# Optimization experiments

Hardware: AMD Instinct MI355X
Metric: run time of the kernel (lower is better)

## Reference

```python
import jax, jax.numpy as jnp
import numpy as np

B, T, S, K, H, V = 8, 100, 400, 8, 512, 32000

def setup_inputs() -> dict:
    key = jax.random.key(0)
    ks = jax.random.split(key, 8)
    return {
        "dec_out": jax.random.normal(ks[0], (B, T, H), jnp.float32),
        "W": jax.random.normal(ks[1], (H, V), jnp.float32) * (1.0 / np.sqrt(H)),
        "b": jnp.zeros((V,), jnp.float32),
        "weights": jax.random.uniform(ks[2], (B, T, S), jnp.float32),
        "p_trans": jax.random.uniform(ks[3], (B, T, 1), jnp.float32),
        "trans_probs": jax.random.uniform(ks[4], (B, S, K), jnp.float32),
        "probs": jax.random.uniform(ks[5], (B, S, K), jnp.float32),
        "idxes": jax.random.randint(ks[6], (B, S, K), 0, V, jnp.int64),
    }

def reference(dec_out, W, b, weights, p_trans, trans_probs, probs, idxes):
    # Generator: linear + softmax over vocab -> (B, T, V)
    scores = jax.nn.softmax(jnp.einsum('bth,hv->btv', dec_out, W) + b, axis=-1)
    # Mask translation probs where source prob <= 0.05
    tp = trans_probs * (probs > 0.05).astype(trans_probs.dtype)  # (B, S, K)
    # scatter_add along vocab dim: tmp[b, s, idxes[b, s, k]] += tp[b, s, k]
    bi = jnp.arange(B)[:, None, None]
    si = jnp.arange(S)[None, :, None]
    tmp = jnp.zeros((B, S, V), dec_out.dtype).at[bi, si, idxes].add(tp)
    # blend copy distribution through attention weights
    trans_scores = jnp.einsum('bts,bsv->btv', weights, tmp)
    return jnp.log(p_trans * trans_scores + (1.0 - p_trans) * scores)
```

## Files before the change

### kernel.cpp

```cpp
#include <hip/hip_runtime.h>

#define Bdim 8
#define Tdim 100
#define Sdim 400
#define Kk   8
#define Hdim 512
#define Vdim 32000
#define Mdim 800
#define VHALF 16000

typedef __attribute__((ext_vector_type(8))) short short8;
typedef __attribute__((ext_vector_type(4))) float float4_t;

static __device__ __forceinline__ unsigned short f2bf(float f) {
    unsigned int x = __float_as_uint(f);
    return (unsigned short)((x + 0x7fffu + ((x >> 16) & 1u)) >> 16);
}
static __device__ __forceinline__ float bf2f(unsigned short h) {
    return __uint_as_float(((unsigned int)h) << 16);
}

static __device__ __forceinline__ void gload_lds16(const void* g, void* s) {
    __builtin_amdgcn_global_load_lds((const __attribute__((address_space(1))) void*)g,
                                     (__attribute__((address_space(3))) void*)s, 16, 0, 0);
}

__global__ void zero_kernel(float* __restrict__ p, int n) {
    int i = blockIdx.x * blockDim.x + threadIdx.x;
    if (i < n) p[i] = 0.f;
}

__global__ void convert_a_kernel(const float* __restrict__ A, unsigned short* __restrict__ Abf, int n) {
    int i = blockIdx.x * blockDim.x + threadIdx.x;
    if (i < n) Abf[i] = f2bf(A[i]);
}

__global__ void transpose_kernel(const float* __restrict__ W, unsigned short* __restrict__ WT) {
    __shared__ float tile[32][33];
    int k0 = blockIdx.y * 32;
    int v0 = blockIdx.x * 32;
    int tx = threadIdx.x & 31;
    int ty = threadIdx.x >> 5;
#pragma unroll
    for (int i = 0; i < 32; i += 8)
        tile[ty + i][tx] = W[(k0 + ty + i) * Vdim + v0 + tx];
    __syncthreads();
#pragma unroll
    for (int i = 0; i < 32; i += 8) {
        int v = v0 + ty + i;
        WT[v * Hdim + k0 + tx] = f2bf(tile[tx][ty + i]);
    }
}

__global__ __launch_bounds__(256) void gemm_kernel(const unsigned short* __restrict__ Abf,
                                                   const unsigned short* __restrict__ WT,
                                                   const float* __restrict__ bias,
                                                   unsigned short* __restrict__ logitsbf,
                                                   float* __restrict__ rowsum) {
    __shared__ __align__(16) unsigned short As[128 * 64];
    __shared__ __align__(16) unsigned short Bs[128 * 64];

    const int tid  = threadIdx.x;
    const int lane = tid & 63;
    const int wave = tid >> 6;
    const int l15  = lane & 15;
    const int kq   = lane >> 4;
    const int m_blk = blockIdx.x * 128;
    const int n_blk = blockIdx.y * 128;
    const int wm = wave & 1, wn = wave >> 1;
    const int m0 = wm * 64, n0 = wn * 64;

    const unsigned short* agp[4];
    const unsigned short* bgp[4];
    unsigned short* alp[4];
    unsigned short* blp[4];
#pragma unroll
    for (int q = 0; q < 4; ++q) {
        int chunk = (q * 4 + wave) * 64 + lane;
        int row = chunk >> 3, c = chunk & 7;
        int gc  = c ^ (row & 7);
        int arow = m_blk + row;
        if (arow >= Mdim) arow = Mdim - 1;
        agp[q] = Abf + (size_t)arow * Hdim + gc * 8;
        bgp[q] = WT + (size_t)(n_blk + row) * Hdim + gc * 8;
        alp[q] = As + (q * 4 + wave) * 512;
        blp[q] = Bs + (q * 4 + wave) * 512;
    }

    int a_off[2][4], b_off[2][4];
#pragma unroll
    for (int ks = 0; ks < 2; ++ks)
#pragma unroll
        for (int i = 0; i < 4; ++i) {
            int ra = m0 + i * 16 + l15;
            a_off[ks][i] = ra * 64 + (((ks * 4 + kq) ^ (ra & 7)) * 8);
            int rb = n0 + i * 16 + l15;
            b_off[ks][i] = rb * 64 + (((ks * 4 + kq) ^ (rb & 7)) * 8);
        }

    float4_t acc[4][4] = {};

    for (int kt = 0; kt < 8; ++kt) {
        if (kt) __syncthreads();
        const int ko = kt * 64;
#pragma unroll
        for (int q = 0; q < 4; ++q) {
            gload_lds16(agp[q] + ko, alp[q]);
            gload_lds16(bgp[q] + ko, blp[q]);
        }
        __syncthreads();
#pragma unroll
        for (int ks = 0; ks < 2; ++ks) {
            short8 af[4], bfr[4];
#pragma unroll
            for (int i = 0; i < 4; ++i) af[i]  = *(const short8*)(As + a_off[ks][i]);
#pragma unroll
            for (int j = 0; j < 4; ++j) bfr[j] = *(const short8*)(Bs + b_off[ks][j]);
#pragma unroll
            for (int i = 0; i < 4; ++i)
#pragma unroll
                for (int j = 0; j < 4; ++j)
                    acc[i][j] = __builtin_amdgcn_mfma_f32_16x16x32_bf16(af[i], bfr[j], acc[i][j], 0, 0, 0);
        }
    }

    float bj[4];
#pragma unroll
    for (int j = 0; j < 4; ++j) bj[j] = bias[n_blk + n0 + j * 16 + l15];

#pragma unroll
    for (int i = 0; i < 4; ++i) {
        float se[4] = {0.f, 0.f, 0.f, 0.f};
        int grow0 = m_blk + m0 + i * 16 + kq * 4;
#pragma unroll
        for (int j = 0; j < 4; ++j) {
            int col = n_blk + n0 + j * 16 + l15;
#pragma unroll
            for (int r = 0; r < 4; ++r) {
                float v = acc[i][j][r] + bj[j];
                se[r] += __expf(v);
                if (grow0 + r < Mdim)
                    logitsbf[(size_t)(grow0 + r) * Vdim + col] = f2bf(v);
            }
        }
#pragma unroll
        for (int r = 0; r < 4; ++r) {
#pragma unroll
            for (int off = 8; off; off >>= 1)
                se[r] += __shfl_xor(se[r], off, 64);
        }
        if (l15 == 0) {
#pragma unroll
            for (int r = 0; r < 4; ++r)
                if (grow0 + r < Mdim) atomicAdd(&rowsum[grow0 + r], se[r]);
        }
    }
}

__global__ __launch_bounds__(512) void combine_kernel(const unsigned short* __restrict__ logitsbf,
                                                      const float* __restrict__ weights,
                                                      const float* __restrict__ p_trans,
                                                      const float* __restrict__ trans_probs,
                                                      const float* __restrict__ probs,
                                                      const int* __restrict__ idxes,
                                                      const float* __restrict__ rowsum,
                                                      float* __restrict__ out) {
    __shared__ __align__(16) float ts[VHALF];

    int bt = blockIdx.x;
    int b  = bt / Tdim;
    int tid = threadIdx.x;

    float pt = p_trans[bt];
    float c1 = (1.f - pt) / rowsum[bt];

    const short8* lrow8 = (const short8*)(logitsbf + (size_t)bt * Vdim);
    float4* out4 = (float4*)(out + (size_t)bt * Vdim);
    float4* ts4  = (float4*)ts;

    for (int h = 0; h < 2; ++h) {
        float4 z = make_float4(0.f, 0.f, 0.f, 0.f);
        for (int i = tid; i < VHALF / 4; i += 512) ts4[i] = z;
        __syncthreads();

        for (int i = tid; i < Sdim * Kk; i += 512) {
            float pv  = probs[b * (Sdim * Kk) + i];
            float tpv = trans_probs[b * (Sdim * Kk) + i];
            int   idx = idxes[b * (Sdim * Kk) + i];
            int   rel = idx - h * VHALF;
            if (pv > 0.05f && (unsigned)rel < (unsigned)VHALF) {
                float w = weights[bt * Sdim + (i >> 3)];
                atomicAdd(&ts[rel], w * tpv);
            }
        }
        __syncthreads();

        for (int i = tid; i < VHALF / 8; i += 512) {
            short8 x8 = lrow8[h * (VHALF / 8) + i];
            float4 t0 = ts4[i * 2];
            float4 t1 = ts4[i * 2 + 1];
            float4 o0, o1;
            o0.x = __logf(pt * t0.x + c1 * __expf(bf2f((unsigned short)x8[0])));
            o0.y = __logf(pt * t0.y + c1 * __expf(bf2f((unsigned short)x8[1])));
            o0.z = __logf(pt * t0.z + c1 * __expf(bf2f((unsigned short)x8[2])));
            o0.w = __logf(pt * t0.w + c1 * __expf(bf2f((unsigned short)x8[3])));
            o1.x = __logf(pt * t1.x + c1 * __expf(bf2f((unsigned short)x8[4])));
            o1.y = __logf(pt * t1.y + c1 * __expf(bf2f((unsigned short)x8[5])));
            o1.z = __logf(pt * t1.z + c1 * __expf(bf2f((unsigned short)x8[6])));
            o1.w = __logf(pt * t1.w + c1 * __expf(bf2f((unsigned short)x8[7])));
            out4[(h * (VHALF / 8) + i) * 2]     = o0;
            out4[(h * (VHALF / 8) + i) * 2 + 1] = o1;
        }
        __syncthreads();
    }
}

extern "C" void kernel_launch(void* const* d_in, const int* in_sizes, int n_in,
                              void* d_out, int out_size, void* d_ws, size_t ws_size,
                              hipStream_t stream) {
    const float* dec_out     = (const float*)d_in[0];
    const float* W           = (const float*)d_in[1];
    const float* bias        = (const float*)d_in[2];
    const float* weights     = (const float*)d_in[3];
    const float* p_trans     = (const float*)d_in[4];
    const float* trans_probs = (const float*)d_in[5];
    const float* probs       = (const float*)d_in[6];
    const int*   idxes       = (const int*)d_in[7];
    float* out = (float*)d_out;

    char* wsb = (char*)d_ws;
    unsigned short* Abf      = (unsigned short*)wsb;
    unsigned short* WT       = (unsigned short*)(wsb + (1ull << 20));
    unsigned short* logitsbf = (unsigned short*)(wsb + (35ull << 20));
    float*          rowsum   = (float*)(wsb + (90ull << 20));

    zero_kernel<<<dim3(4), dim3(256), 0, stream>>>(rowsum, Mdim);
    convert_a_kernel<<<dim3((Mdim * Hdim + 255) / 256), dim3(256), 0, stream>>>(dec_out, Abf, Mdim * Hdim);
    transpose_kernel<<<dim3(Vdim / 32, Hdim / 32), dim3(256), 0, stream>>>(W, WT);
    gemm_kernel<<<dim3(7, Vdim / 128), dim3(256), 0, stream>>>(Abf, WT, bias, logitsbf, rowsum);
    combine_kernel<<<dim3(Mdim), dim3(512), 0, stream>>>(logitsbf, weights, p_trans, trans_probs,
                                                         probs, idxes, rowsum, out);
}
```

Before: 293.2 us.

## Double-buffer GEMM LDS tiles, remap workgroups per XCD, vectorize convert and transpose

The GEMM now keeps two LDS buffers, so the next K-tile is loaded from global memory while the current one feeds the MFMAs. This removes one barrier per iteration and hides load latency, at the cost of doubling LDS use, which may lower occupancy. Workgroups are launched on a 1D grid and remapped so that consecutive tiles land on the same XCD, aiming for better L2 reuse of the shared A and W tiles. The dec_out conversion and the W transpose now use float4 loads and 64x64 tiles with 16-byte bf16 stores, cutting the number of memory transactions in these preprocessing kernels.

New measurement: 284.7 us. 2.9% less time.

```diff
diff --git a/kernel.cpp b/kernel.cpp
--- a/kernel.cpp
+++ b/kernel.cpp
@@ -10,6 +10,7 @@
 #define VHALF 16000
 
 typedef __attribute__((ext_vector_type(8))) short short8;
+typedef __attribute__((ext_vector_type(4))) short short4v;
 typedef __attribute__((ext_vector_type(4))) float float4_t;
 
 static __device__ __forceinline__ unsigned short f2bf(float f) {
@@ -30,25 +31,42 @@
     if (i < n) p[i] = 0.f;
 }
 
-__global__ void convert_a_kernel(const float* __restrict__ A, unsigned short* __restrict__ Abf, int n) {
+__global__ void convert_a_kernel(const float* __restrict__ A, unsigned short* __restrict__ Abf, int n4) {
     int i = blockIdx.x * blockDim.x + threadIdx.x;
-    if (i < n) Abf[i] = f2bf(A[i]);
-}
-
-__global__ void transpose_kernel(const float* __restrict__ W, unsigned short* __restrict__ WT) {
-    __shared__ float tile[32][33];
-    int k0 = blockIdx.y * 32;
-    int v0 = blockIdx.x * 32;
-    int tx = threadIdx.x & 31;
-    int ty = threadIdx.x >> 5;
-#pragma unroll
-    for (int i = 0; i < 32; i += 8)
-        tile[ty + i][tx] = W[(k0 + ty + i) * Vdim + v0 + tx];
+    if (i < n4) {
+        float4 f = ((const float4*)A)[i];
+        short4v s;
+        s[0] = (short)f2bf(f.x); s[1] = (short)f2bf(f.y);
+        s[2] = (short)f2bf(f.z); s[3] = (short)f2bf(f.w);
+        *(short4v*)(Abf + i * 4) = s;
+    }
+}
+
+__global__ __launch_bounds__(256) void transpose_kernel(const float* __restrict__ W,
+                                                        unsigned short* __restrict__ WT) {
+    __shared__ float tile[64][65];
+    const int k0 = blockIdx.y * 64;
+    const int v0 = blockIdx.x * 64;
+    const int t  = threadIdx.x;
+    const int tx = t & 15;
+    const int ty = t >> 4;
+#pragma unroll
+    for (int i = 0; i < 64; i += 16) {
+        float4 f = *(const float4*)&W[(size_t)(k0 + ty + i) * Vdim + v0 + tx * 4];
+        tile[ty + i][tx * 4 + 0] = f.x;
+        tile[ty + i][tx * 4 + 1] = f.y;
+        tile[ty + i][tx * 4 + 2] = f.z;
+        tile[ty + i][tx * 4 + 3] = f.w;
+    }
     __syncthreads();
-#pragma unroll
-    for (int i = 0; i < 32; i += 8) {
-        int v = v0 + ty + i;
-        WT[v * Hdim + k0 + tx] = f2bf(tile[tx][ty + i]);
+    const int c = t & 7;
+    const int v = t >> 3;
+#pragma unroll
+    for (int i = 0; i < 64; i += 32) {
+        short8 s;
+#pragma unroll
+        for (int j = 0; j < 8; ++j) s[j] = (short)f2bf(tile[c * 8 + j][v + i]);
+        *(short8*)&WT[(size_t)(v0 + v + i) * Hdim + k0 + c * 8] = s;
     }
 }
 
@@ -57,23 +75,30 @@
                                                    const float* __restrict__ bias,
                                                    unsigned short* __restrict__ logitsbf,
                                                    float* __restrict__ rowsum) {
-    __shared__ __align__(16) unsigned short As[128 * 64];
-    __shared__ __align__(16) unsigned short Bs[128 * 64];
+    __shared__ __align__(16) unsigned short As[2 * 128 * 64];
+    __shared__ __align__(16) unsigned short Bs[2 * 128 * 64];
 
     const int tid  = threadIdx.x;
     const int lane = tid & 63;
     const int wave = tid >> 6;
     const int l15  = lane & 15;
     const int kq   = lane >> 4;
-    const int m_blk = blockIdx.x * 128;
-    const int n_blk = blockIdx.y * 128;
+
+    const int NWG = 7 * 250;
+    const int orig = blockIdx.x;
+    const int xcd = orig & 7;
+    const int q8  = NWG >> 3;
+    const int r8  = NWG & 7;
+    const int wg  = (xcd < r8 ? xcd * (q8 + 1) : r8 * (q8 + 1) + (xcd - r8) * q8) + (orig >> 3);
+    const int m_blk = (wg % 7) * 128;
+    const int n_blk = (wg / 7) * 128;
+
     const int wm = wave & 1, wn = wave >> 1;
     const int m0 = wm * 64, n0 = wn * 64;
 
     const unsigned short* agp[4];
     const unsigned short* bgp[4];
-    unsigned short* alp[4];
-    unsigned short* blp[4];
+    int lslot[4];
 #pragma unroll
     for (int q = 0; q < 4; ++q) {
         int chunk = (q * 4 + wave) * 64 + lane;
@@ -83,8 +108,7 @@
         if (arow >= Mdim) arow = Mdim - 1;
         agp[q] = Abf + (size_t)arow * Hdim + gc * 8;
         bgp[q] = WT + (size_t)(n_blk + row) * Hdim + gc * 8;
-        alp[q] = As + (q * 4 + wave) * 512;
-        blp[q] = Bs + (q * 4 + wave) * 512;
+        lslot[q] = (q * 4 + wave) * 512;
     }
 
     int a_off[2][4], b_off[2][4];
@@ -100,27 +124,43 @@
 
     float4_t acc[4][4] = {};
 
+#pragma unroll
+    for (int q = 0; q < 4; ++q) {
+        gload_lds16(agp[q], As + lslot[q]);
+        gload_lds16(bgp[q], Bs + lslot[q]);
+    }
+    __syncthreads();
+
+    int cur = 0;
+#pragma unroll
     for (int kt = 0; kt < 8; ++kt) {
-        if (kt) __syncthreads();
-        const int ko = kt * 64;
-#pragma unroll
-        for (int q = 0; q < 4; ++q) {
-            gload_lds16(agp[q] + ko, alp[q]);
-            gload_lds16(bgp[q] + ko, blp[q]);
-        }
-        __syncthreads();
+        if (kt < 7) {
+            const int ko = (kt + 1) * 64;
+            const int nb = (cur ^ 1) * 8192;
+#pragma unroll
+            for (int q = 0; q < 4; ++q) {
+                gload_lds16(agp[q] + ko, As + nb + lslot[q]);
+                gload_lds16(bgp[q] + ko, Bs + nb + lslot[q]);
+            }
+        }
+        const unsigned short* Ab = As + cur * 8192;
+        const unsigned short* Bb = Bs + cur * 8192;
 #pragma unroll
         for (int ks = 0; ks < 2; ++ks) {
             short8 af[4], bfr[4];
 #pragma unroll
-            for (int i = 0; i < 4; ++i) af[i]  = *(const short8*)(As + a_off[ks][i]);
-#pragma unroll
-            for (int j = 0; j < 4; ++j) bfr[j] = *(const short8*)(Bs + b_off[ks][j]);
+            for (int i = 0; i < 4; ++i) af[i]  = *(const short8*)(Ab + a_off[ks][i]);
+#pragma unroll
+            for (int j = 0; j < 4; ++j) bfr[j] = *(const short8*)(Bb + b_off[ks][j]);
 #pragma unroll
             for (int i = 0; i < 4; ++i)
 #pragma unroll
                 for (int j = 0; j < 4; ++j)
                     acc[i][j] = __builtin_amdgcn_mfma_f32_16x16x32_bf16(af[i], bfr[j], acc[i][j], 0, 0, 0);
+        }
+        if (kt < 7) {
+            __syncthreads();
+            cur ^= 1;
         }
     }
 
@@ -235,9 +275,9 @@
     float*          rowsum   = (float*)(wsb + (90ull << 20));
 
     zero_kernel<<<dim3(4), dim3(256), 0, stream>>>(rowsum, Mdim);
-    convert_a_kernel<<<dim3((Mdim * Hdim + 255) / 256), dim3(256), 0, stream>>>(dec_out, Abf, Mdim * Hdim);
-    transpose_kernel<<<dim3(Vdim / 32, Hdim / 32), dim3(256), 0, stream>>>(W, WT);
-    gemm_kernel<<<dim3(7, Vdim / 128), dim3(256), 0, stream>>>(Abf, WT, bias, logitsbf, rowsum);
+    convert_a_kernel<<<dim3((Mdim * Hdim / 4 + 255) / 256), dim3(256), 0, stream>>>(dec_out, Abf, Mdim * Hdim / 4);
+    transpose_kernel<<<dim3(Vdim / 64, Hdim / 64), dim3(256), 0, stream>>>(W, WT);
+    gemm_kernel<<<dim3(7 * (Vdim / 128)), dim3(256), 0, stream>>>(Abf, WT, bias, logitsbf, rowsum);
     combine_kernel<<<dim3(Mdim), dim3(512), 0, stream>>>(logitsbf, weights, p_trans, trans_probs,
                                                          probs, idxes, rowsum, out);
 }
```
